# Kernel tuning notes

Measured on AMD Instinct MI355X. Metric: run time of the kernel, lower is better.

Reference implementation:

```python
import jax, jax.numpy as jnp
import numpy as np

N = 500_000          # number of particles
D = 6                # phase-space dimension
N_BINS = 128         # bins per axis
SQRT2 = 1.4142135623730951
BANDWIDTH = 1.0      # kernel width relative to bin width (module default)


def setup_inputs() -> dict:
    key = jax.random.key(0)
    x = jax.random.normal(key, (N, D), dtype=jnp.float32)
    edges = jnp.linspace(-3.0, 3.0, N_BINS + 1, dtype=jnp.float32)
    return {"x": x, "bin_edges_x": edges, "bin_edges_y": edges}


def _cdf_weights(u, edges, bw):
    """Per-point Gaussian mass in each bin via CDF (erf) differences.

    u: (n,), edges: (m+1,) -> weights (n, m); row sums <= 1.
    """
    z = jax.scipy.special.erf((edges[None, :] - u[:, None]) / (bw * SQRT2))  # (n, m+1)
    return 0.5 * (z[:, 1:] - z[:, :-1])  # (n, m)


def reference(x, bin_edges_x, bin_edges_y):
    dx = bin_edges_x[1] - bin_edges_x[0]
    dy = bin_edges_y[1] - bin_edges_y[0]
    bw_x = BANDWIDTH * dx
    bw_y = BANDWIDTH * dy
    # axis = (0, 1): project onto first two phase-space coordinates
    wx = _cdf_weights(x[:, 0], bin_edges_x, bw_x)  # (n, bx)
    wy = _cdf_weights(x[:, 1], bin_edges_y, bw_y)  # (n, by)
    hist = jnp.einsum('ni,nj->ij', wx, wy)         # (bx, by)
    # normalize to a probability density over the grid
    hist = hist / (hist.sum() * dx * dy)
    return hist
```

## Files before the change

kernel.cpp:

```cpp
#include <hip/hip_runtime.h>
#include <math.h>


#define NBINS   128
#define NB2     (NBINS * NBINS)
#define KC      128
#define AX_B    16384
#define THREADS 1024
#define NBLOCKS 512
#define QSCALE  320.0f

typedef int i32x4 __attribute__((ext_vector_type(4)));

static __device__ __forceinline__ unsigned short f2bf(float f) {
    unsigned int b = __float_as_uint(f);
    b += 0x7fff + ((b >> 16) & 1);
    return (unsigned short)(b >> 16);
}
static __device__ __forceinline__ float bf2f(unsigned short u) {
    return __uint_as_float((unsigned int)u << 16);
}

static __device__ __forceinline__ float erf_fast(float x) {
    const float ax = fabsf(x);
    const float t  = __builtin_amdgcn_rcpf(fmaf(0.3275911f, ax, 1.0f));
    const float e  = __expf(-x * x);
    float p = fmaf(1.061405429f, t, -1.453152027f);
    p = fmaf(p, t, 1.421413741f);
    p = fmaf(p, t, -0.284496736f);
    p = fmaf(p, t, 0.254829592f);
    p = p * t;
    return copysignf(fmaf(-p, e, 1.0f), x);
}

__global__ __launch_bounds__(THREADS, 8) void hist_mfma_kernel(
    const float* __restrict__ x,
    const float* __restrict__ edges_x,
    const float* __restrict__ edges_y,
    unsigned short* __restrict__ partials,
    float* __restrict__ btot,
    int n)
{
    __shared__ __align__(16) signed char sh[2 * AX_B];
    __shared__ int xw[16];

    const int tid  = threadIdx.x;
    const int lane = tid & 63;
    const int wv   = tid >> 6;

    const float e0x = edges_x[0];
    const float dxw = edges_x[1] - e0x;
    const float e0y = edges_y[0];
    const float dyw = edges_y[1] - e0y;

    const bool isrole = (wv < 4);
    const int axis = (tid >> 7) & 1;
    const int pl   = tid & 127;
    const float e0   = axis ? e0y : e0x;
    const float invd = 1.0f / (axis ? dyw : dxw);
    const float cc   = 0.7071067811865476f;
    signed char* const sdst =
        sh + axis * AX_B + (pl >> 6) * 1024 + ((pl >> 4) & 3) * 256 + (pl & 15);

    const int rowT = (wv & 3) * 2;
    const int colT = (wv >> 2) * 2;

    i32x4 acc[2][2];
    #pragma unroll
    for (int i = 0; i < 2; ++i)
        #pragma unroll
        for (int j = 0; j < 2; ++j)
            acc[i][j] = (i32x4){0, 0, 0, 0};

    const int nchunks = (n + KC - 1) / KC;

    int b0 = 0, oldb0 = 0;
    signed char qv[8];
    if (isrole) {
        float u = 1e30f;
        const int p = blockIdx.x * KC + pl;
        if (blockIdx.x < nchunks && p < n) u = x[(size_t)p * 6 + axis];
        const float spos = (u - e0) * invd;
        int b = (int)floorf(spos + 0.5f) - 4;
        b0 = b < 0 ? 0 : (b > NBINS - 8 ? NBINS - 8 : b);
        const float t0 = ((float)b0 - spos) * cc;
        float z[9];
        #pragma unroll
        for (int k = 0; k < 9; ++k) z[k] = erf_fast(t0 + (float)k * cc);
        #pragma unroll
        for (int k = 0; k < 8; ++k)
            qv[k] = (signed char)(int)rintf(0.5f * (z[k + 1] - z[k]) * QSCALE);
        oldb0 = b0;
    }

    {
        float4* zp = (float4*)sh;
        zp[tid] = (float4){0.f, 0.f, 0.f, 0.f};
        zp[tid + THREADS] = (float4){0.f, 0.f, 0.f, 0.f};
    }
    __syncthreads();

    for (int chunk = blockIdx.x; chunk < nchunks; chunk += gridDim.x) {
        if (isrole) {
            #pragma unroll
            for (int k = 0; k < 8; ++k) {
                const int b = oldb0 + k;
                sdst[(b >> 4) * 2048 + (b & 15) * 16] = 0;
            }
            #pragma unroll
            for (int k = 0; k < 8; ++k) {
                const int b = b0 + k;
                sdst[(b >> 4) * 2048 + (b & 15) * 16] = qv[k];
            }
        }
        __syncthreads();

        float un = 1e30f;
        const int nchunk = chunk + gridDim.x;
        if (isrole && nchunk < nchunks) {
            const int pn = nchunk * KC + pl;
            if (pn < n) un = x[(size_t)pn * 6 + axis];
        }

        #pragma unroll
        for (int s = 0; s < 2; ++s) {
            i32x4 av[2];
            #pragma unroll
            for (int i = 0; i < 2; ++i)
                av[i] = *(const i32x4*)(sh + (rowT + i) * 2048 + s * 1024 + lane * 16);
            #pragma unroll
            for (int j = 0; j < 2; ++j) {
                const i32x4 bv = *(const i32x4*)(sh + AX_B + (colT + j) * 2048 + s * 1024 + lane * 16);
                #pragma unroll
                for (int i = 0; i < 2; ++i)
                    acc[i][j] = __builtin_amdgcn_mfma_i32_16x16x64_i8(
                        av[i], bv, acc[i][j], 0, 0, 0);
            }
        }

        if (isrole) {
            oldb0 = b0;
            const float spos = (un - e0) * invd;
            int b = (int)floorf(spos + 0.5f) - 4;
            b0 = b < 0 ? 0 : (b > NBINS - 8 ? NBINS - 8 : b);
            const float t0 = ((float)b0 - spos) * cc;
            float z[9];
            #pragma unroll
            for (int k = 0; k < 9; ++k) z[k] = erf_fast(t0 + (float)k * cc);
            #pragma unroll
            for (int k = 0; k < 8; ++k)
                qv[k] = (signed char)(int)rintf(0.5f * (z[k + 1] - z[k]) * QSCALE);
        }
        __syncthreads();
    }

    int bsum = 0;
    {
        const float qs = 1.0f / (QSCALE * QSCALE);
        unsigned short* my = partials + (size_t)blockIdx.x * NB2;
        const int r0 = (lane >> 4) * 4;
        const int c0 = lane & 15;
        #pragma unroll
        for (int i = 0; i < 2; ++i)
            #pragma unroll
            for (int j = 0; j < 2; ++j)
                #pragma unroll
                for (int g = 0; g < 4; ++g) {
                    const int v = acc[i][j][g];
                    bsum += v;
                    const int row = (rowT + i) * 16 + r0 + g;
                    const int col = (colT + j) * 16 + c0;
                    my[row * NBINS + col] = f2bf((float)v * qs);
                }
    }
    #pragma unroll
    for (int off = 32; off > 0; off >>= 1) bsum += __shfl_down(bsum, off, 64);
    if (lane == 0) xw[wv] = bsum;
    __syncthreads();
    if (tid == 0) {
        const float qs = 1.0f / (QSCALE * QSCALE);
        int s = 0;
        #pragma unroll
        for (int k = 0; k < 16; ++k) s += xw[k];
        btot[blockIdx.x] = (float)s * qs;
    }
}

__global__ void reduce_kernel(const unsigned short* __restrict__ partials,
                              const float* __restrict__ btot,
                              const float* __restrict__ edges_x,
                              const float* __restrict__ edges_y,
                              float* __restrict__ out)
{
    __shared__ float4 red[16][16];
    __shared__ float ws[4];
    __shared__ float stot;

    const int t = threadIdx.x;
    const int bin4 = t & 15;
    const int pg = t >> 4;
    const int binBase = blockIdx.x * 64;

    float tl = btot[t] + btot[t + 256];
    #pragma unroll
    for (int off = 32; off > 0; off >>= 1) tl += __shfl_down(tl, off, 64);
    if ((t & 63) == 0) ws[t >> 6] = tl;

    const unsigned short* p =
        partials + (size_t)(pg * 32) * NB2 + binBase + bin4 * 4;
    float4 s = {0.f, 0.f, 0.f, 0.f};
    #pragma unroll 8
    for (int k = 0; k < 32; ++k) {
        const ushort4 v = *(const ushort4*)(p + (size_t)k * NB2);
        s.x += bf2f(v.x); s.y += bf2f(v.y); s.z += bf2f(v.z); s.w += bf2f(v.w);
    }
    red[pg][bin4] = s;
    __syncthreads();

    if (t == 0) {
        const float dxw = edges_x[1] - edges_x[0];
        const float dyw = edges_y[1] - edges_y[0];
        stot = 1.0f / ((ws[0] + ws[1] + ws[2] + ws[3]) * dxw * dyw);
    }
    __syncthreads();

    if (t < 16) {
        float4 a = red[0][t];
        #pragma unroll
        for (int g = 1; g < 16; ++g) {
            const float4 b = red[g][t];
            a.x += b.x; a.y += b.y; a.z += b.z; a.w += b.w;
        }
        a.x *= stot; a.y *= stot; a.z *= stot; a.w *= stot;
        *(float4*)(out + binBase + t * 4) = a;
    }
}

extern "C" void kernel_launch(void* const* d_in, const int* in_sizes, int n_in,
                              void* d_out, int out_size, void* d_ws, size_t ws_size,
                              hipStream_t stream)
{
    const float* x  = (const float*)d_in[0];
    const float* ex = (const float*)d_in[1];
    const float* ey = (const float*)d_in[2];
    float* out = (float*)d_out;
    const int n = in_sizes[0] / 6;

    unsigned short* partials = (unsigned short*)d_ws;
    float* btot = (float*)((char*)d_ws + (size_t)NBLOCKS * NB2 * 2);

    hist_mfma_kernel<<<NBLOCKS, THREADS, 0, stream>>>(x, ex, ey, partials, btot, n);
    reduce_kernel<<<NB2 / 64, 256, 0, stream>>>(partials, btot, ex, ey, out);
}
```

Measured before the change: 85.12 us.

## Replace int8 MFMA dense outer-product with sparse LDS atomic 8x8 scatter

Drops the int8 MFMA approach, which multiplied mostly-zero 128-bin weight vectors per chunk of particles. Each thread now computes its particle's 8 nonzero quantized weights per axis and atomically adds the 64 products into a padded per-block int histogram in shared memory. This removes the dense matrix work and per-chunk barriers, but adds 64 LDS atomics per particle, a large LDS footprint (~66KB) that limits occupancy, and possible contention in the central bins.

```diff
diff --git a/kernel.cpp b/kernel.cpp
--- a/kernel.cpp
+++ b/kernel.cpp
@@ -4,13 +4,10 @@
 
 #define NBINS   128
 #define NB2     (NBINS * NBINS)
-#define KC      128
-#define AX_B    16384
-#define THREADS 1024
+#define LDH     129
+#define THREADS 512
 #define NBLOCKS 512
 #define QSCALE  320.0f
-
-typedef int i32x4 __attribute__((ext_vector_type(4)));
 
 static __device__ __forceinline__ unsigned short f2bf(float f) {
     unsigned int b = __float_as_uint(f);
@@ -33,7 +30,23 @@
     return copysignf(fmaf(-p, e, 1.0f), x);
 }
 
-__global__ __launch_bounds__(THREADS, 8) void hist_mfma_kernel(
+static __device__ __forceinline__ void axis_q(
+    float u, float e0, float inv, int& b0, int q[8])
+{
+    const float cc = 0.7071067811865476f;
+    const float spos = (u - e0) * inv;
+    int b = (int)floorf(spos + 0.5f) - 4;
+    b0 = b < 0 ? 0 : (b > NBINS - 8 ? NBINS - 8 : b);
+    const float t0 = ((float)b0 - spos) * cc;
+    float z[9];
+    #pragma unroll
+    for (int k = 0; k < 9; ++k) z[k] = erf_fast(t0 + (float)k * cc);
+    #pragma unroll
+    for (int k = 0; k < 8; ++k)
+        q[k] = (int)rintf(0.5f * (z[k + 1] - z[k]) * QSCALE);
+}
+
+__global__ __launch_bounds__(THREADS, 4) void hist_sparse_kernel(
     const float* __restrict__ x,
     const float* __restrict__ edges_x,
     const float* __restrict__ edges_y,
@@ -41,138 +54,65 @@
     float* __restrict__ btot,
     int n)
 {
-    __shared__ __align__(16) signed char sh[2 * AX_B];
-    __shared__ int xw[16];
+    __shared__ int lh[NBINS * LDH];
+    __shared__ int xw[8];
 
     const int tid  = threadIdx.x;
     const int lane = tid & 63;
     const int wv   = tid >> 6;
 
+    for (int i = tid; i < NBINS * LDH; i += THREADS) lh[i] = 0;
+
     const float e0x = edges_x[0];
     const float dxw = edges_x[1] - e0x;
     const float e0y = edges_y[0];
     const float dyw = edges_y[1] - e0y;
+    const float ivx = 1.0f / dxw;
+    const float ivy = 1.0f / dyw;
+    __syncthreads();
 
-    const bool isrole = (wv < 4);
-    const int axis = (tid >> 7) & 1;
-    const int pl   = tid & 127;
-    const float e0   = axis ? e0y : e0x;
-    const float invd = 1.0f / (axis ? dyw : dxw);
-    const float cc   = 0.7071067811865476f;
-    signed char* const sdst =
-        sh + axis * AX_B + (pl >> 6) * 1024 + ((pl >> 4) & 3) * 256 + (pl & 15);
+    int bsum = 0;
+    const int stride = gridDim.x * THREADS;
+    for (int p = blockIdx.x * THREADS + tid; p < n; p += stride) {
+        const float2 u = *(const float2*)(x + (size_t)p * 6);
+        int bx0, by0, qx[8], qy[8];
+        axis_q(u.x, e0x, ivx, bx0, qx);
+        axis_q(u.y, e0y, ivy, by0, qy);
 
-    const int rowT = (wv & 3) * 2;
-    const int colT = (wv >> 2) * 2;
+        int sx = 0, sy = 0;
+        #pragma unroll
+        for (int k = 0; k < 8; ++k) { sx += qx[k]; sy += qy[k]; }
+        bsum += sx * sy;
 
-    i32x4 acc[2][2];
-    #pragma unroll
-    for (int i = 0; i < 2; ++i)
+        int* const base = lh + bx0 * LDH + by0;
         #pragma unroll
-        for (int j = 0; j < 2; ++j)
-            acc[i][j] = (i32x4){0, 0, 0, 0};
-
-    const int nchunks = (n + KC - 1) / KC;
-
-    int b0 = 0, oldb0 = 0;
-    signed char qv[8];
-    if (isrole) {
-        float u = 1e30f;
-        const int p = blockIdx.x * KC + pl;
-        if (blockIdx.x < nchunks && p < n) u = x[(size_t)p * 6 + axis];
-        const float spos = (u - e0) * invd;
-        int b = (int)floorf(spos + 0.5f) - 4;
-        b0 = b < 0 ? 0 : (b > NBINS - 8 ? NBINS - 8 : b);
-        const float t0 = ((float)b0 - spos) * cc;
-        float z[9];
-        #pragma unroll
-        for (int k = 0; k < 9; ++k) z[k] = erf_fast(t0 + (float)k * cc);
-        #pragma unroll
-        for (int k = 0; k < 8; ++k)
-            qv[k] = (signed char)(int)rintf(0.5f * (z[k + 1] - z[k]) * QSCALE);
-        oldb0 = b0;
-    }
-
-    {
-        float4* zp = (float4*)sh;
-        zp[tid] = (float4){0.f, 0.f, 0.f, 0.f};
-        zp[tid + THREADS] = (float4){0.f, 0.f, 0.f, 0.f};
+        for (int i = 0; i < 8; ++i) {
+            const int qi = qx[i];
+            #pragma unroll
+            for (int j = 0; j < 8; ++j)
+                atomicAdd(base + i * LDH + j, qi * qy[j]);
+        }
     }
     __syncthreads();
 
-    for (int chunk = blockIdx.x; chunk < nchunks; chunk += gridDim.x) {
-        if (isrole) {
-            #pragma unroll
-            for (int k = 0; k < 8; ++k) {
-                const int b = oldb0 + k;
-                sdst[(b >> 4) * 2048 + (b & 15) * 16] = 0;
-            }
-            #pragma unroll
-            for (int k = 0; k < 8; ++k) {
-                const int b = b0 + k;
-                sdst[(b >> 4) * 2048 + (b & 15) * 16] = qv[k];
-            }
-        }
-        __syncthreads();
-
-        float un = 1e30f;
-        const int nchunk = chunk + gridDim.x;
-        if (isrole && nchunk < nchunks) {
-            const int pn = nchunk * KC + pl;
-            if (pn < n) un = x[(size_t)pn * 6 + axis];
-        }
-
-        #pragma unroll
-        for (int s = 0; s < 2; ++s) {
-            i32x4 av[2];
-            #pragma unroll
-            for (int i = 0; i < 2; ++i)
-                av[i] = *(const i32x4*)(sh + (rowT + i) * 2048 + s * 1024 + lane * 16);
-            #pragma unroll
-            for (int j = 0; j < 2; ++j) {
-                const i32x4 bv = *(const i32x4*)(sh + AX_B + (colT + j) * 2048 + s * 1024 + lane * 16);
-                #pragma unroll
-                for (int i = 0; i < 2; ++i)
-                    acc[i][j] = __builtin_amdgcn_mfma_i32_16x16x64_i8(
-                        av[i], bv, acc[i][j], 0, 0, 0);
-            }
-        }
-
-        if (isrole) {
-            oldb0 = b0;
-            const float spos = (un - e0) * invd;
-            int b = (int)floorf(spos + 0.5f) - 4;
-            b0 = b < 0 ? 0 : (b > NBINS - 8 ? NBINS - 8 : b);
-            const float t0 = ((float)b0 - spos) * cc;
-            float z[9];
-            #pragma unroll
-            for (int k = 0; k < 9; ++k) z[k] = erf_fast(t0 + (float)k * cc);
-            #pragma unroll
-            for (int k = 0; k < 8; ++k)
-                qv[k] = (signed char)(int)rintf(0.5f * (z[k + 1] - z[k]) * QSCALE);
-        }
-        __syncthreads();
-    }
-
-    int bsum = 0;
     {
         const float qs = 1.0f / (QSCALE * QSCALE);
         unsigned short* my = partials + (size_t)blockIdx.x * NB2;
-        const int r0 = (lane >> 4) * 4;
-        const int c0 = lane & 15;
         #pragma unroll
-        for (int i = 0; i < 2; ++i)
-            #pragma unroll
-            for (int j = 0; j < 2; ++j)
-                #pragma unroll
-                for (int g = 0; g < 4; ++g) {
-                    const int v = acc[i][j][g];
-                    bsum += v;
-                    const int row = (rowT + i) * 16 + r0 + g;
-                    const int col = (colT + j) * 16 + c0;
-                    my[row * NBINS + col] = f2bf((float)v * qs);
-                }
+        for (int v = 0; v < 8; ++v) {
+            const int e = tid * 32 + v * 4;
+            const int r = e >> 7;
+            const int c = e & 127;
+            const int* row = lh + r * LDH + c;
+            ushort4 o;
+            o.x = f2bf((float)row[0] * qs);
+            o.y = f2bf((float)row[1] * qs);
+            o.z = f2bf((float)row[2] * qs);
+            o.w = f2bf((float)row[3] * qs);
+            *(ushort4*)(my + e) = o;
+        }
     }
+
     #pragma unroll
     for (int off = 32; off > 0; off >>= 1) bsum += __shfl_down(bsum, off, 64);
     if (lane == 0) xw[wv] = bsum;
@@ -181,7 +121,7 @@
         const float qs = 1.0f / (QSCALE * QSCALE);
         int s = 0;
         #pragma unroll
-        for (int k = 0; k < 16; ++k) s += xw[k];
+        for (int k = 0; k < 8; ++k) s += xw[k];
         btot[blockIdx.x] = (float)s * qs;
     }
 }
@@ -249,6 +189,6 @@
     unsigned short* partials = (unsigned short*)d_ws;
     float* btot = (float*)((char*)d_ws + (size_t)NBLOCKS * NB2 * 2);
 
-    hist_mfma_kernel<<<NBLOCKS, THREADS, 0, stream>>>(x, ex, ey, partials, btot, n);
+    hist_sparse_kernel<<<NBLOCKS, THREADS, 0, stream>>>(x, ex, ey, partials, btot, n);
     reduce_kernel<<<NB2 / 64, 256, 0, stream>>>(partials, btot, ex, ey, out);
 }
```

Measured after the change: 81.91 us. 3.8% less time.
